# Kernel optimization log

Hardware: AMD Instinct MI355X
Metric: run time of the kernel (lower is better)

## Reference

```python
import jax, jax.numpy as jnp
import numpy as np

B, DIM, KEY_DIM, NH, AR, RES, KS = 32, 512, 16, 8, 4, 64, 5
D = AR * KEY_DIM          # 64, per-head value dim
C4 = DIM // 4             # 128, q/k channel dim
CHUNK = DIM // NH         # 64, per-head input chunk
SCALE = KEY_DIM ** -0.5


def setup_inputs() -> dict:
    key = jax.random.key(0)
    ks = jax.random.split(key, 8)
    def rn(k, shape, fan):
        return jax.random.normal(k, shape, jnp.float32) * (fan ** -0.5)
    x = jax.random.normal(ks[0], (B, DIM, RES, RES), jnp.float32)
    qk_w = rn(ks[1], (DIM // 2, DIM), DIM)            # fused 1x1 conv+BN weight
    qk_b = jnp.zeros((DIM // 2,), jnp.float32)
    dws_w = rn(ks[2], (C4, 1, KS, KS), KS * KS)        # depthwise conv weight
    dws_b = jnp.zeros((C4,), jnp.float32)
    vs_w = rn(ks[3], (NH, D, CHUNK), CHUNK)            # per-head 1x1 conv weights
    vs_b = jnp.zeros((NH, D), jnp.float32)
    proj_w = rn(ks[4], (DIM, D * NH), D * NH)
    proj_b = jnp.zeros((DIM,), jnp.float32)
    bias_h = jax.random.normal(ks[5], (1, RES), jnp.float32) * 0.02
    bias_w = jax.random.normal(ks[6], (1, RES), jnp.float32) * 0.02
    # offset id for (p1, p2) is exactly |p1 - p2| given enumeration order
    idx = jnp.abs(jnp.arange(RES)[:, None] - jnp.arange(RES)[None, :]).astype(jnp.int32)
    return dict(x=x, qk_w=qk_w, qk_b=qk_b, dws_w=dws_w, dws_b=dws_b,
                vs_w=vs_w, vs_b=vs_b, proj_w=proj_w, proj_b=proj_b,
                bias_h=bias_h, bias_w=bias_w, idx_h=idx, idx_w=idx)


def reference(x, qk_w, qk_b, dws_w, dws_b, vs_w, vs_b, proj_w, proj_b,
              bias_h, bias_w, idx_h, idx_w):
    ab_h = bias_h[0][idx_h]                               # [N, N]
    ab_w = bias_w[0][idx_w]                               # [N, N]
    # qk: fused 1x1 conv + BN -> [B, C/2, H, W]
    feat = jnp.einsum('oc,bchw->bohw', qk_w, x) + qk_b[None, :, None, None]
    q, k = feat[:, :C4], feat[:, C4:]
    # depthwise 5x5 conv on q
    q = jax.lax.conv_general_dilated(
        q, dws_w, (1, 1), 'SAME',
        dimension_numbers=('NCHW', 'OIHW', 'NCHW'),
        feature_group_count=C4) + dws_b[None, :, None, None]
    qr_w = jnp.transpose(q, (0, 2, 3, 1))                 # [B, H, W, C4]
    kr_w = jnp.transpose(k, (0, 2, 3, 1))                 # [B, H, W, C4]
    attn_w = jax.nn.softmax(
        jnp.einsum('bhqc,bhkc->bhqk', qr_w, kr_w) * SCALE + ab_w, axis=-1)
    qr_h = jnp.transpose(qr_w, (0, 2, 1, 3))              # [B, W, H, C4]
    kr_h = jnp.transpose(kr_w, (0, 2, 1, 3))
    attn_h = jax.nn.softmax(
        jnp.einsum('bwqc,bwkc->bwqk', qr_h, kr_h) * SCALE + ab_h, axis=-1)
    # cascaded per-head value chain
    feats_out = []
    feat_i = x[:, :CHUNK]
    for i in range(NH):
        if i > 0:
            feat_i = feat_i + x[:, i * CHUNK:(i + 1) * CHUNK]
        v = jnp.einsum('dc,bchw->bdhw', vs_w[i], feat_i) + vs_b[i][None, :, None, None]
        v = jnp.transpose(v, (0, 2, 3, 1))                # [B, H, W, d]
        v = jnp.einsum('bhqk,bhkd->bhqd', attn_w, v)      # attend along W
        v = jnp.transpose(v, (0, 2, 1, 3))                # [B, W, H, d]
        f = jnp.einsum('bwqk,bwkd->bwqd', attn_h, v)      # attend along H
        feats_out.append(jnp.transpose(f, (0, 3, 2, 1)))  # [B, d, H, W]
    out = jnp.concatenate(feats_out, axis=1)              # [B, d*NH, H, W]
    out = jax.nn.relu(out)
    out = jnp.einsum('oc,bchw->bohw', proj_w, out) + proj_b[None, :, None, None]
    return out
```

## Files before the change

### kernel.cpp

```cpp
#include <hip/hip_runtime.h>

#define PIX 4096
#define SCALE 0.25f

typedef _Float16 f16x8 __attribute__((ext_vector_type(8)));
typedef _Float16 f16x4 __attribute__((ext_vector_type(4)));
typedef float f32x4 __attribute__((ext_vector_type(4)));

__device__ inline void gload_lds16(const _Float16* g, _Float16* l) {
  __builtin_amdgcn_global_load_lds((const __attribute__((address_space(1))) void*)g,
                                   (__attribute__((address_space(3))) void*)l, 16, 0, 0);
}

__global__ __launch_bounds__(256) void k_cvt(const float* __restrict__ in,
                                             _Float16* __restrict__ out, int n) {
  int i = blockIdx.x * 256 + threadIdx.x;
  if (i < n) out[i] = (_Float16)in[i];
}

__global__ __launch_bounds__(256) void k_build_wbig(const float* __restrict__ vs_w,
                                                    _Float16* __restrict__ Wbig) {
  int row = blockIdx.x;
  int i = row >> 6, d = row & 63;
  for (int col = threadIdx.x; col < 512; col += 256) {
    int j = col >> 6, c = col & 63;
    Wbig[row * 512 + col] = (j <= i) ? (_Float16)vs_w[i * 4096 + d * 64 + c] : (_Float16)0;
  }
}

__global__ __launch_bounds__(256) void k_xt(const float* __restrict__ x,
                                            _Float16* __restrict__ xh) {
  __shared__ float tile[64][65];
  int b = blockIdx.z, k0 = blockIdx.y * 64, p0 = blockIdx.x * 64;
  const float* xp = x + ((size_t)b * 512 + k0) * PIX + p0;
  _Float16* out = xh + (size_t)b * PIX * 512;
  int t = threadIdx.x;
  int r = t >> 4, c4 = (t & 15) << 2;
#pragma unroll
  for (int it = 0; it < 4; ++it) {
    float4 v = *(const float4*)&xp[(size_t)(r + it * 16) * PIX + c4];
    tile[r + it * 16][c4 + 0] = v.x; tile[r + it * 16][c4 + 1] = v.y;
    tile[r + it * 16][c4 + 2] = v.z; tile[r + it * 16][c4 + 3] = v.w;
  }
  __syncthreads();
  int pr = t >> 5, kk = (t & 31) << 1;
#pragma unroll
  for (int it = 0; it < 8; ++it) {
    int p = pr + it * 8;
    union { _Float16 h[2]; unsigned int u; } pk;
    pk.h[0] = (_Float16)tile[kk][p]; pk.h[1] = (_Float16)tile[kk + 1][p];
    *(unsigned int*)&out[(size_t)(p0 + p) * 512 + k0 + kk] = pk.u;
  }
}

template<int MODE>
__global__ __launch_bounds__(512, 2) void k_mg8(const _Float16* __restrict__ A,
                                                const _Float16* __restrict__ B,
                                                const float* __restrict__ bias,
                                                const _Float16* __restrict__ attn,
                                                float* C, _Float16* H, _Float16* H2,
                                                int nwg_m) {
  constexpr int MROWS = (MODE == 1) ? 128 : 256;
  constexpr int AH = MROWS * 32;
  constexpr int SLOT = AH + 8192;
  constexpr int MI = MROWS / 32;
  __shared__ __align__(16) _Float16 lds[65536];
  int nwg = gridDim.x;
  int id = blockIdx.x;
  int qq = nwg >> 3;
  id = (id & 7) * qq + (id >> 3);
  int mb = id % nwg_m;
  int rest = id / nwg_m;
  int pb = rest & 15;
  int b  = rest >> 4;
  int m0 = mb * MROWS, p0 = pb * 256;
  int t = threadIdx.x, wid = t >> 6, lane = t & 63;
  int wm = wid >> 2, wn = wid & 3;
  int lr = lane & 15, q4 = lane >> 4;
  const _Float16* Ab = A + (size_t)m0 * 512;
  const _Float16* Bp = B + (size_t)b * 2097152 + (size_t)p0 * 512;

  int nt = (MODE == 1) ? ((m0 + 128) >> 6) : 8;
  int nsub = nt * 2;

  auto STAGE = [&](int g) {
    int slot = g & 3;
    _Float16* dA = lds + slot * SLOT;
    _Float16* dB = dA + AH;
    size_t ks = (size_t)g * 32;
    if constexpr (MODE == 1) {
      int L = wid * 64 + lane;
      int row = L >> 2, sl = L & 3;
      int c = sl ^ ((row >> 1) & 3);
      gload_lds16(Ab + (size_t)row * 512 + ks + c * 8, dA + (size_t)(wid * 64) * 8);
    } else {
#pragma unroll
      for (int is = 0; is < 2; ++is) {
        int L = is * 512 + wid * 64 + lane;
        int row = L >> 2, sl = L & 3;
        int c = sl ^ ((row >> 1) & 3);
        gload_lds16(Ab + (size_t)row * 512 + ks + c * 8, dA + (size_t)(is * 512 + wid * 64) * 8);
      }
    }
#pragma unroll
    for (int is = 0; is < 2; ++is) {
      int L = is * 512 + wid * 64 + lane;
      int row = L >> 2, sl = L & 3;
      int c = sl ^ ((row >> 1) & 3);
      gload_lds16(Bp + (size_t)row * 512 + ks + c * 8, dB + (size_t)(is * 512 + wid * 64) * 8);
    }
  };

  f32x4 acc[MI][4] = {};
  STAGE(0); STAGE(1); STAGE(2);
  for (int n = 0; n < nsub; ++n) {
    if (n + 3 < nsub) STAGE(n + 3);
    int r = nsub - 1 - n; if (r > 3) r = 3;
    if constexpr (MODE == 1) {
      if (r == 3)      asm volatile("s_waitcnt vmcnt(9)" ::: "memory");
      else if (r == 2) asm volatile("s_waitcnt vmcnt(6)" ::: "memory");
      else if (r == 1) asm volatile("s_waitcnt vmcnt(3)" ::: "memory");
      else             asm volatile("s_waitcnt vmcnt(0)" ::: "memory");
    } else {
      if (r == 3)      asm volatile("s_waitcnt vmcnt(12)" ::: "memory");
      else if (r == 2) asm volatile("s_waitcnt vmcnt(8)" ::: "memory");
      else if (r == 1) asm volatile("s_waitcnt vmcnt(4)" ::: "memory");
      else             asm volatile("s_waitcnt vmcnt(0)" ::: "memory");
    }
    __builtin_amdgcn_s_barrier();
    const _Float16* A_s = lds + (n & 3) * SLOT;
    const _Float16* B_s = A_s + AH;
    f16x8 af[MI], bf[4];
#pragma unroll
    for (int mi = 0; mi < MI; ++mi) {
      int row = wm * (MROWS / 2) + mi * 16 + lr;
      af[mi] = *(const f16x8*)&A_s[row * 32 + ((q4 ^ ((row >> 1) & 3)) << 3)];
    }
#pragma unroll
    for (int ni = 0; ni < 4; ++ni) {
      int row = wn * 64 + ni * 16 + lr;
      bf[ni] = *(const f16x8*)&B_s[row * 32 + ((q4 ^ ((row >> 1) & 3)) << 3)];
    }
    __builtin_amdgcn_s_setprio(1);
#pragma unroll
    for (int mi = 0; mi < MI; ++mi)
#pragma unroll
      for (int ni = 0; ni < 4; ++ni)
        acc[mi][ni] = __builtin_amdgcn_mfma_f32_16x16x32_f16(af[mi], bf[ni], acc[mi][ni], 0, 0, 0);
    __builtin_amdgcn_s_setprio(0);
    __builtin_amdgcn_s_barrier();
  }

  if (MODE == 0) {
#pragma unroll
    for (int mi = 0; mi < MI; ++mi)
#pragma unroll
      for (int rr = 0; rr < 4; ++rr) {
        int m = m0 + wm * 128 + mi * 16 + q4 * 4 + rr;
        float bi = bias[m];
        float* crow = C + ((size_t)b * 512 + m) * PIX + p0 + wn * 64;
#pragma unroll
        for (int ni = 0; ni < 4; ++ni)
          crow[ni * 16 + lr] = acc[mi][ni][rr] + bi;
      }
  }

  if (MODE == 1) {
    _Float16* Cs = lds + wid * 4096;
#pragma unroll
    for (int mi = 0; mi < 4; ++mi)
#pragma unroll
      for (int ni = 0; ni < 4; ++ni)
#pragma unroll
        for (int rr = 0; rr < 4; ++rr) {
          int row = mi * 16 + q4 * 4 + rr;
          int col = ni * 16 + lr;
          Cs[row * 64 + ((((col >> 3) ^ (row & 7)) << 3) | (col & 7))] =
              (_Float16)(acc[mi][ni][rr] + bias[m0 + wm * 64 + row]);
        }
    int s = pb * 4 + wn;
    const _Float16* Ab2 = attn + ((size_t)b * 64 + s) * 4096;
    f16x8 bfr[4][2];
#pragma unroll
    for (int ni = 0; ni < 4; ++ni)
#pragma unroll
      for (int kk = 0; kk < 2; ++kk)
        bfr[ni][kk] = *(const f16x8*)&Ab2[(ni * 16 + lr) * 64 + q4 * 8 + kk * 32];
    f32x4 acc2[4][4] = {};
#pragma unroll
    for (int mi2 = 0; mi2 < 4; ++mi2)
#pragma unroll
      for (int kk = 0; kk < 2; ++kk) {
        int row = mi2 * 16 + lr;
        f16x8 afr = *(const f16x8*)&Cs[row * 64 + (((q4 + kk * 4) ^ (row & 7)) << 3)];
#pragma unroll
        for (int ni2 = 0; ni2 < 4; ++ni2)
          acc2[mi2][ni2] = __builtin_amdgcn_mfma_f32_16x16x32_f16(afr, bfr[ni2][kk], acc2[mi2][ni2], 0, 0, 0);
      }
#pragma unroll
    for (int mi2 = 0; mi2 < 4; ++mi2)
#pragma unroll
      for (int rr = 0; rr < 4; ++rr) {
        int m = m0 + wm * 64 + mi2 * 16 + q4 * 4 + rr;
        _Float16* crow = H + ((size_t)b * 512 + m) * PIX + p0 + wn * 64;
#pragma unroll
        for (int ni2 = 0; ni2 < 4; ++ni2)
          crow[ni2 * 16 + lr] = (_Float16)acc2[mi2][ni2][rr];
      }
  }

  if (MODE == 2) {
    if (wm == 0) {
#pragma unroll
      for (int mi = 0; mi < MI; ++mi)
#pragma unroll
        for (int rr = 0; rr < 4; ++rr) {
          int m = mi * 16 + q4 * 4 + rr;
          float bi = bias[m];
          _Float16* crow = H2 + ((size_t)b * 128 + m) * PIX + p0 + wn * 64;
#pragma unroll
          for (int ni = 0; ni < 4; ++ni)
            crow[ni * 16 + lr] = (_Float16)(acc[mi][ni][rr] + bi);
        }
    } else {
      _Float16* Ls = lds + (size_t)(wid - 4) * 16384;
#pragma unroll
      for (int mi = 0; mi < MI; ++mi)
#pragma unroll
        for (int ni = 0; ni < 4; ++ni)
#pragma unroll
          for (int rr = 0; rr < 4; ++rr) {
            int ch = mi * 16 + q4 * 4 + rr;
            Ls[(ni * 16 + lr) * 136 + ch] = (_Float16)(acc[mi][ni][rr] + bias[128 + ch]);
          }
      _Float16* khb = H + ((size_t)b * PIX + p0 + wn * 64) * 128;
#pragma unroll
      for (int it = 0; it < 16; ++it) {
        int chk = it * 64 + lane;
        int prow = chk >> 4, cc = (chk & 15) << 3;
        *(f16x8*)&khb[(size_t)prow * 128 + cc] = *(const f16x8*)&Ls[prow * 136 + cc];
      }
    }
  }
}

__global__ __launch_bounds__(256) void k_dwconv(const _Float16* __restrict__ feat,
                                                const float* __restrict__ w,
                                                const float* __restrict__ bias,
                                                _Float16* __restrict__ qc) {
  __shared__ float tile[68][68];
  int c = blockIdx.x, b = blockIdx.y;
  const _Float16* in = feat + ((size_t)b * 128 + c) * PIX;
  float wreg[25];
#pragma unroll
  for (int i = 0; i < 25; ++i) wreg[i] = w[c * 25 + i];
  float bi = bias[c];
  int t = threadIdx.x;
  for (int idx = t; idx < 68 * 68; idx += 256) {
    int y = idx / 68, xx = idx - y * 68;
    int h = y - 2, ww = xx - 2;
    float v = 0.f;
    if (h >= 0 && h < 64 && ww >= 0 && ww < 64) v = (float)in[h * 64 + ww];
    tile[y][xx] = v;
  }
  __syncthreads();
  _Float16* out = qc + ((size_t)b * 128 + c) * PIX;
  int tx = (t & 15) << 2, ty = (t >> 4) << 2;
#pragma unroll
  for (int i = 0; i < 4; ++i) {
    f16x4 o;
#pragma unroll
    for (int j = 0; j < 4; ++j) {
      float s = bi;
#pragma unroll
      for (int dy = 0; dy < 5; ++dy)
#pragma unroll
        for (int dx = 0; dx < 5; ++dx)
          s += wreg[dy * 5 + dx] * tile[ty + i + dy][tx + j + dx];
      o[j] = (_Float16)s;
    }
    *(f16x4*)&out[(ty + i) * 64 + tx] = o;
  }
}

__global__ __launch_bounds__(256) void k_qkt16(const _Float16* __restrict__ in,
                                               _Float16* __restrict__ out) {
  __shared__ __align__(16) _Float16 Ts[64 * 136];
  int p0 = blockIdx.x * 64, b = blockIdx.y;
  const _Float16* ip = in + (size_t)b * 128 * PIX;
  int t = threadIdx.x;
#pragma unroll
  for (int it = 0; it < 4; ++it) {
    int i4 = it * 256 + t;
    int c = i4 >> 3, pc = (i4 & 7) << 3;
    f16x8 v = *(const f16x8*)&ip[(size_t)c * PIX + p0 + pc];
#pragma unroll
    for (int j = 0; j < 8; ++j) Ts[(pc + j) * 136 + c] = v[j];
  }
  __syncthreads();
  _Float16* op = out + (size_t)b * (PIX * 128) + (size_t)p0 * 128;
#pragma unroll
  for (int it = 0; it < 4; ++it) {
    int ch = it * 256 + t;
    int p = ch >> 4, cc = (ch & 15) << 3;
    *(f16x8*)&op[p * 128 + cc] = *(const f16x8*)&Ts[p * 136 + cc];
  }
}

__global__ __launch_bounds__(256) void k_mattn(const _Float16* __restrict__ qh,
                                               const _Float16* __restrict__ kh,
                                               const float* __restrict__ bias_w,
                                               const float* __restrict__ bias_h,
                                               _Float16* __restrict__ attnW,
                                               _Float16* __restrict__ attnH) {
  __shared__ __align__(16) _Float16 Qs[64 * 136];
  __shared__ __align__(16) _Float16 Ks[64 * 136];
  __shared__ float bl[64];
  int j = blockIdx.x, b = blockIdx.y, which = blockIdx.z;
  const float* bias = which ? bias_h : bias_w;
  _Float16* attn = which ? attnH : attnW;
  int t = threadIdx.x;
  if (t < 64) bl[t] = bias[t];
  const _Float16* qb = qh + (size_t)b * (PIX * 128);
  const _Float16* kb = kh + (size_t)b * (PIX * 128);
#pragma unroll
  for (int it = 0; it < 4; ++it) {
    int idx = it * 256 + t;
    int r = idx >> 4, cc = (idx & 15) << 3;
    size_t p = which ? (size_t)(j + 64 * r) : (size_t)(j * 64 + r);
    *(f16x8*)&Qs[r * 136 + cc] = *(const f16x8*)&qb[p * 128 + cc];
    *(f16x8*)&Ks[r * 136 + cc] = *(const f16x8*)&kb[p * 128 + cc];
  }
  __syncthreads();
  int wave = t >> 6, lane = t & 63;
  int lr = lane & 15, q4 = lane >> 4;
  f16x8 af[4];
#pragma unroll
  for (int kk = 0; kk < 4; ++kk)
    af[kk] = *(const f16x8*)&Qs[(wave * 16 + lr) * 136 + q4 * 8 + kk * 32];
  f32x4 acc[4] = {};
#pragma unroll
  for (int ni = 0; ni < 4; ++ni)
#pragma unroll
    for (int kk = 0; kk < 4; ++kk) {
      f16x8 bf = *(const f16x8*)&Ks[(ni * 16 + lr) * 136 + q4 * 8 + kk * 32];
      acc[ni] = __builtin_amdgcn_mfma_f32_16x16x32_f16(af[kk], bf, acc[ni], 0, 0, 0);
    }
  float ev[4][4], sm[4];
#pragma unroll
  for (int r = 0; r < 4; ++r) {
    int qrow = wave * 16 + q4 * 4 + r;
    float m = -1e30f;
#pragma unroll
    for (int ni = 0; ni < 4; ++ni) {
      int k = ni * 16 + lr;
      ev[ni][r] = acc[ni][r] * SCALE + bl[abs(qrow - k)];
      m = fmaxf(m, ev[ni][r]);
    }
    m = fmaxf(m, __shfl_xor(m, 1)); m = fmaxf(m, __shfl_xor(m, 2));
    m = fmaxf(m, __shfl_xor(m, 4)); m = fmaxf(m, __shfl_xor(m, 8));
    float s = 0.f;
#pragma unroll
    for (int ni = 0; ni < 4; ++ni) { ev[ni][r] = __expf(ev[ni][r] - m); s += ev[ni][r]; }
    s += __shfl_xor(s, 1); s += __shfl_xor(s, 2);
    s += __shfl_xor(s, 4); s += __shfl_xor(s, 8);
    sm[r] = 1.f / s;
  }
  _Float16* ab = attn + (((size_t)b * 64 + j) * 64) * 64;
#pragma unroll
  for (int r = 0; r < 4; ++r) {
    int qrow = wave * 16 + q4 * 4 + r;
#pragma unroll
    for (int ni = 0; ni < 4; ++ni)
      ab[qrow * 64 + ni * 16 + lr] = (_Float16)(ev[ni][r] * sm[r]);
  }
}

__global__ __launch_bounds__(256) void k_hmix(const _Float16* __restrict__ tT,
                                              const _Float16* __restrict__ attnH,
                                              _Float16* __restrict__ ght) {
  __shared__ __align__(16) _Float16 Ts[128 * 64];
  __shared__ __align__(16) _Float16 Ls[64 * 136];
  int id = blockIdx.x;
  int ct = id & 3, w = (id >> 2) & 63, b = id >> 8;
  int t = threadIdx.x, wid = t >> 6, lane = t & 63;
  int lr = lane & 15, q4 = lane >> 4;
  const _Float16* Tb = tT + ((size_t)b * 512 + ct * 128) * PIX + w * 64;
#pragma unroll
  for (int it = 0; it < 4; ++it) {
    int idx = it * 256 + t;
    int row = idx >> 3, c = idx & 7;
    int sc = c ^ (row & 7);
    gload_lds16(Tb + (size_t)row * PIX + sc * 8, &Ts[(it * 256 + wid * 64) * 8]);
  }
  const _Float16* Ab = attnH + ((size_t)b * 64 + w) * 4096;
  f16x8 bfr[4][2];
#pragma unroll
  for (int ni = 0; ni < 4; ++ni)
#pragma unroll
    for (int kk = 0; kk < 2; ++kk)
      bfr[ni][kk] = *(const f16x8*)&Ab[(ni * 16 + lr) * 64 + q4 * 8 + kk * 32];
  __syncthreads();
  f32x4 acc[2][4] = {};
#pragma unroll
  for (int mi = 0; mi < 2; ++mi) {
    int rr = wid * 32 + mi * 16 + lr;
#pragma unroll
    for (int kk = 0; kk < 2; ++kk) {
      f16x8 af = *(const f16x8*)&Ts[rr * 64 + (((q4 + 4 * kk) ^ (rr & 7)) << 3)];
#pragma unroll
      for (int ni = 0; ni < 4; ++ni)
        acc[mi][ni] = __builtin_amdgcn_mfma_f32_16x16x32_f16(af, bfr[ni][kk], acc[mi][ni], 0, 0, 0);
    }
  }
#pragma unroll
  for (int mi = 0; mi < 2; ++mi)
#pragma unroll
    for (int ni = 0; ni < 4; ++ni)
#pragma unroll
      for (int rr = 0; rr < 4; ++rr) {
        float v = acc[mi][ni][rr];
        Ls[(ni * 16 + lr) * 136 + wid * 32 + mi * 16 + q4 * 4 + rr] =
            (_Float16)(v > 0.f ? v : 0.f);
      }
  __syncthreads();
  _Float16* gb = ght + (size_t)b * PIX * 512 + ct * 128;
#pragma unroll
  for (int it = 0; it < 4; ++it) {
    int idx = it * 256 + t;
    int hp = idx >> 4, cc = (idx & 15) << 3;
    *(f16x8*)&gb[((size_t)hp * 64 + w) * 512 + cc] = *(const f16x8*)&Ls[hp * 136 + cc];
  }
}

__global__ __launch_bounds__(256) void k_t16(const _Float16* __restrict__ in,
                                             _Float16* __restrict__ out) {
  __shared__ _Float16 tile[64][65];
  int img = blockIdx.x;
  const _Float16* ip = in + (size_t)img * PIX;
  _Float16* op = out + (size_t)img * PIX;
  int t = threadIdx.x;
  int col = t & 63, r0 = t >> 6;
  for (int it = 0; it < 16; ++it) {
    int r = r0 + it * 4;
    tile[r][col] = ip[r * 64 + col];
  }
  __syncthreads();
  for (int it = 0; it < 16; ++it) {
    int r = r0 + it * 4;
    op[r * 64 + col] = tile[col][r];
  }
}

extern "C" void kernel_launch(void* const* d_in, const int* in_sizes, int n_in,
                              void* d_out, int out_size, void* d_ws, size_t ws_size,
                              hipStream_t stream) {
  const float* x      = (const float*)d_in[0];
  const float* qk_w   = (const float*)d_in[1];
  const float* qk_b   = (const float*)d_in[2];
  const float* dws_w  = (const float*)d_in[3];
  const float* dws_b  = (const float*)d_in[4];
  const float* vs_w   = (const float*)d_in[5];
  const float* vs_b   = (const float*)d_in[6];
  const float* proj_w = (const float*)d_in[7];
  const float* proj_b = (const float*)d_in[8];
  const float* bias_h = (const float*)d_in[9];
  const float* bias_w = (const float*)d_in[10];

  float* ws = (float*)d_ws;
  float* dout = (float*)d_out;

  _Float16* xh    = (_Float16*)ws;
  _Float16* ght   = xh;
  _Float16* tT    = (_Float16*)(ws + 33554432);
  _Float16* attnW = (_Float16*)(ws + 67108864);
  _Float16* attnH = (_Float16*)(ws + 71303168);
  _Float16* qkw_h  = (_Float16*)(ws + 75497472);
  _Float16* wbig_h = (_Float16*)(ws + 75563008);
  _Float16* pjw_h  = (_Float16*)(ws + 75694080);

  _Float16* feat_h = (_Float16*)dout;
  _Float16* qc_h   = (_Float16*)(dout + 8388608);
  _Float16* qh     = (_Float16*)(dout + 16777216);
  _Float16* kh     = (_Float16*)(dout + 25165824);
  _Float16* Vh     = (_Float16*)(dout + 33554432);

  k_cvt<<<dim3(512), 256, 0, stream>>>(qk_w, qkw_h, 131072);
  k_cvt<<<dim3(1024), 256, 0, stream>>>(proj_w, pjw_h, 262144);
  k_build_wbig<<<512, 256, 0, stream>>>(vs_w, wbig_h);
  k_xt<<<dim3(64, 8, 32), 256, 0, stream>>>(x, xh);
  k_mg8<2><<<512, 512, 0, stream>>>(qkw_h, xh, qk_b, nullptr, nullptr, kh, feat_h, 1);
  k_dwconv<<<dim3(128, 32), 256, 0, stream>>>(feat_h, dws_w, dws_b, qc_h);
  k_qkt16<<<dim3(64, 32), 256, 0, stream>>>(qc_h, qh);
  k_mattn<<<dim3(64, 32, 2), 256, 0, stream>>>(qh, kh, bias_w, bias_h, attnW, attnH);
  k_mg8<1><<<2048, 512, 0, stream>>>(wbig_h, xh, vs_b, attnW, nullptr, Vh, nullptr, 4);
  k_t16<<<32 * 512, 256, 0, stream>>>(Vh, tT);
  k_hmix<<<8192, 256, 0, stream>>>(tT, attnH, ght);
  k_mg8<0><<<1024, 512, 0, stream>>>(pjw_h, ght, proj_b, nullptr, dout, nullptr, nullptr, 2);
}
```

Measured before the change: 599.8 us.

## Shrink LDS pipeline depth for value/proj GEMMs to raise occupancy; fuse prep kernels

For the MODE 0 and MODE 1 GEMM variants, the LDS staging pipeline drops from four slots (three stages in flight) to double buffering with one stage ahead. LDS per block shrinks to 64 KB and the launch bound asks for four workgroups per CU, so more waves can hide latency. The waitcnt thresholds are adjusted to match. The three weight-conversion kernels are also merged into one launch to cut launch overhead. The trade-off is less prefetch depth per block, and the higher occupancy target may force register spilling.

Result: slower. 1.263 ms (+110.6%).

```diff
diff --git a/kernel.cpp b/kernel.cpp
--- a/kernel.cpp
+++ b/kernel.cpp
@@ -12,19 +12,19 @@
                                    (__attribute__((address_space(3))) void*)l, 16, 0, 0);
 }
 
-__global__ __launch_bounds__(256) void k_cvt(const float* __restrict__ in,
-                                             _Float16* __restrict__ out, int n) {
+__global__ __launch_bounds__(256) void k_prep(const float* __restrict__ qk_w,
+                                              const float* __restrict__ proj_w,
+                                              const float* __restrict__ vs_w,
+                                              _Float16* __restrict__ qkw_h,
+                                              _Float16* __restrict__ pjw_h,
+                                              _Float16* __restrict__ wbig_h) {
   int i = blockIdx.x * 256 + threadIdx.x;
-  if (i < n) out[i] = (_Float16)in[i];
-}
-
-__global__ __launch_bounds__(256) void k_build_wbig(const float* __restrict__ vs_w,
-                                                    _Float16* __restrict__ Wbig) {
-  int row = blockIdx.x;
-  int i = row >> 6, d = row & 63;
-  for (int col = threadIdx.x; col < 512; col += 256) {
-    int j = col >> 6, c = col & 63;
-    Wbig[row * 512 + col] = (j <= i) ? (_Float16)vs_w[i * 4096 + d * 64 + c] : (_Float16)0;
+  if (i < 131072) qkw_h[i] = (_Float16)qk_w[i];
+  if (i < 262144) {
+    pjw_h[i] = (_Float16)proj_w[i];
+    int row = i >> 9, col = i & 511;
+    int hi = row >> 6, d = row & 63, j = col >> 6, c = col & 63;
+    wbig_h[i] = (j <= hi) ? (_Float16)vs_w[hi * 4096 + d * 64 + c] : (_Float16)0;
   }
 }
 
@@ -54,17 +54,20 @@
 }
 
 template<int MODE>
-__global__ __launch_bounds__(512, 2) void k_mg8(const _Float16* __restrict__ A,
-                                                const _Float16* __restrict__ B,
-                                                const float* __restrict__ bias,
-                                                const _Float16* __restrict__ attn,
-                                                float* C, _Float16* H, _Float16* H2,
-                                                int nwg_m) {
+__global__ __launch_bounds__(512, MODE == 2 ? 2 : 4)
+void k_mg8(const _Float16* __restrict__ A,
+           const _Float16* __restrict__ B,
+           const float* __restrict__ bias,
+           const _Float16* __restrict__ attn,
+           float* C, _Float16* H, _Float16* H2, int nwg_m) {
   constexpr int MROWS = (MODE == 1) ? 128 : 256;
   constexpr int AH = MROWS * 32;
   constexpr int SLOT = AH + 8192;
   constexpr int MI = MROWS / 32;
-  __shared__ __align__(16) _Float16 lds[65536];
+  constexpr int DEPTH = (MODE == 2) ? 3 : 1;
+  constexpr int NSLOT = (MODE == 2) ? 4 : 2;
+  constexpr int LDSH = (MODE == 2) ? NSLOT * SLOT : 32768;
+  __shared__ __align__(16) _Float16 lds[LDSH];
   int nwg = gridDim.x;
   int id = blockIdx.x;
   int qq = nwg >> 3;
@@ -84,7 +87,7 @@
   int nsub = nt * 2;
 
   auto STAGE = [&](int g) {
-    int slot = g & 3;
+    int slot = g % NSLOT;
     _Float16* dA = lds + slot * SLOT;
     _Float16* dB = dA + AH;
     size_t ks = (size_t)g * 32;
@@ -112,15 +115,17 @@
   };
 
   f32x4 acc[MI][4] = {};
-  STAGE(0); STAGE(1); STAGE(2);
+  if constexpr (DEPTH == 3) { STAGE(0); STAGE(1); STAGE(2); }
+  else STAGE(0);
   for (int n = 0; n < nsub; ++n) {
-    if (n + 3 < nsub) STAGE(n + 3);
-    int r = nsub - 1 - n; if (r > 3) r = 3;
+    if (n + DEPTH < nsub) STAGE(n + DEPTH);
+    int r = nsub - 1 - n; if (r > DEPTH) r = DEPTH;
     if constexpr (MODE == 1) {
-      if (r == 3)      asm volatile("s_waitcnt vmcnt(9)" ::: "memory");
-      else if (r == 2) asm volatile("s_waitcnt vmcnt(6)" ::: "memory");
-      else if (r == 1) asm volatile("s_waitcnt vmcnt(3)" ::: "memory");
-      else             asm volatile("s_waitcnt vmcnt(0)" ::: "memory");
+      if (r >= 1) asm volatile("s_waitcnt vmcnt(3)" ::: "memory");
+      else        asm volatile("s_waitcnt vmcnt(0)" ::: "memory");
+    } else if constexpr (MODE == 0) {
+      if (r >= 1) asm volatile("s_waitcnt vmcnt(4)" ::: "memory");
+      else        asm volatile("s_waitcnt vmcnt(0)" ::: "memory");
     } else {
       if (r == 3)      asm volatile("s_waitcnt vmcnt(12)" ::: "memory");
       else if (r == 2) asm volatile("s_waitcnt vmcnt(8)" ::: "memory");
@@ -128,7 +133,7 @@
       else             asm volatile("s_waitcnt vmcnt(0)" ::: "memory");
     }
     __builtin_amdgcn_s_barrier();
-    const _Float16* A_s = lds + (n & 3) * SLOT;
+    const _Float16* A_s = lds + (n % NSLOT) * SLOT;
     const _Float16* B_s = A_s + AH;
     f16x8 af[MI], bf[4];
 #pragma unroll
@@ -485,9 +490,7 @@
   _Float16* kh     = (_Float16*)(dout + 25165824);
   _Float16* Vh     = (_Float16*)(dout + 33554432);
 
-  k_cvt<<<dim3(512), 256, 0, stream>>>(qk_w, qkw_h, 131072);
-  k_cvt<<<dim3(1024), 256, 0, stream>>>(proj_w, pjw_h, 262144);
-  k_build_wbig<<<512, 256, 0, stream>>>(vs_w, wbig_h);
+  k_prep<<<1024, 256, 0, stream>>>(qk_w, proj_w, vs_w, qkw_h, pjw_h, wbig_h);
   k_xt<<<dim3(64, 8, 32), 256, 0, stream>>>(x, xh);
   k_mg8<2><<<512, 512, 0, stream>>>(qkw_h, xh, qk_b, nullptr, nullptr, kh, feat_h, 1);
   k_dwconv<<<dim3(128, 32), 256, 0, stream>>>(feat_h, dws_w, dws_b, qc_h);
```
